# Kernel optimization log

Hardware: AMD Instinct MI355X
Metric: run time of the kernel (lower is better)

The kernel has to match this reference:

```python
import jax, jax.numpy as jnp
import numpy as np

TAU = 0.01          # gumbel_softmax temperature
EPS = 1e-7          # tf.keras.backend.epsilon()
DEPTH = 5
N_NODES = 2 ** DEPTH - 1   # 31 internal nodes
N_LEAVES = 2 ** DEPTH      # 32 leaves


def _build_route():
    # route[l, node + dir*N_NODES] = 1 along the root-to-leaf path of leaf l
    # (same structure old_route_to_new_route produces for a perfect tree)
    route = np.zeros((N_LEAVES, 2 * N_NODES), dtype=np.float32)
    for l in range(N_LEAVES):
        node = 0
        for d in range(DEPTH):
            bit = (l >> (DEPTH - 1 - d)) & 1  # 0 = left, 1 = right
            route[l, node + bit * N_NODES] = 1.0
            node = 2 * node + 1 + bit
    return route


def setup_inputs() -> dict:
    B, F, T = 32768, 128, 100
    key = jax.random.key(0)
    k1, k2, k3, k4 = jax.random.split(key, 4)
    x = jax.random.normal(k1, (B, F), dtype=jnp.float32)
    kernel = jax.random.normal(k2, (T, F, N_NODES), dtype=jnp.float32) * 0.1
    bias = jax.random.normal(k3, (T, N_NODES), dtype=jnp.float32) * 0.1
    leaf = jax.random.normal(k4, (T, N_LEAVES), dtype=jnp.float32)
    route = jnp.asarray(_build_route())  # [L, 2N], shared tree topology
    return {"x": x, "kernel": kernel, "bias": bias, "leaf": leaf, "route": route}


def reference(x, kernel, bias, leaf, route):
    # NodeLayer: matmul(x, concat([K, -K], 1)) + concat([b, -b], 0)
    h = jnp.einsum("bf,tfn->btn", x, kernel) + bias          # [B, T, N]
    h2 = jnp.concatenate([h, -h], axis=-1)                   # [B, T, 2N]
    # activation1: log(clip(sigmoid(clip(h/tau, -32, 32)), eps, 1))
    a1 = jnp.log(jnp.clip(jax.nn.sigmoid(jnp.clip(h2 / TAU, -32.0, 32.0)), EPS, 1.0))
    # route aggregation: sum log-probs along each root->leaf path
    r = jnp.einsum("btm,lm->btl", a1, route)                 # [B, T, L]
    # activation2: exp(clip(., -32, 0)) -> leaf routing probabilities
    probs = jnp.exp(jnp.clip(r, -32.0, 0.0))
    # weight leaf values by route probabilities, sum over leaves and trees
    return jnp.einsum("btl,tl->b", probs, leaf)              # [B] raw GBM output
```

## Files before the change

### kernel.cpp

```cpp
#include <hip/hip_runtime.h>

typedef _Float16 f16x8 __attribute__((ext_vector_type(8)));
typedef float    f32x4 __attribute__((ext_vector_type(4)));
typedef float    f32x2 __attribute__((ext_vector_type(2)));

#define NTREES  100
#define WAVES   8
#define NCH     13
#define BM      32
#define SCALE   144.269504088896f

#define H_OFF   8192
#define LDS_BYTES (H_OFF + WAVES * 4096)

__device__ __forceinline__ float exp2_fast(float v) {
#if __has_builtin(__builtin_amdgcn_exp2f)
  return __builtin_amdgcn_exp2f(v);
#else
  return exp2f(v);
#endif
}

__device__ __forceinline__ void sig2(float z, float& sl, float& sr) {
  z = fmaxf(z, -24.0f);
  float e = exp2_fast(-z);
  sl = __builtin_amdgcn_rcpf(1.0f + e);
  sr = e * sl;
}

__device__ __forceinline__ int node_perm(int sc, float& sg) {
  const int half = sc >> 4, c = sc & 15;
  sg = 1.0f;
  if (c == 0) { if (half) sg = -1.0f; return 0; }
  if (c == 1) return 1 + half;
  if (c < 4)  return 1 + 2 * half + c;
  if (c < 8)  return 3 + 4 * half + c;
  return 7 + 8 * half + c;
}

__global__ void prep_b(const float* __restrict__ kern, const float* __restrict__ bias,
                       unsigned short* __restrict__ bws, float* __restrict__ bias_s) {
  __shared__ float kt[128][33];
  const int t = blockIdx.x, tid = threadIdx.x;
  const float* src = kern + (size_t)t * (128 * 31);
  for (int i = tid; i < 128 * 32; i += 256) {
    const int f = i >> 5, sc = i & 31;
    float sg; const int g = node_perm(sc, sg);
    kt[f][sc] = src[f * 31 + g] * (SCALE * sg);
  }
  if (tid < 32) {
    float sg; const int g = node_perm(tid, sg);
    bias_s[t * 32 + tid] = bias[t * 31 + g] * (SCALE * sg);
  }
  __syncthreads();
  unsigned short* dst = bws + (size_t)t * 4096;
  for (int s = tid; s < 512; s += 256) {
    const int ks = s >> 7, fr = (s >> 6) & 1, lane = s & 63;
    const int n  = (fr << 4) + (lane & 15);
    const int k0 = ks * 32 + ((lane >> 4) << 3);
    f16x8 o;
    #pragma unroll
    for (int j = 0; j < 8; ++j) o[j] = (_Float16)kt[k0 + j][n];
    *(f16x8*)(dst + s * 8) = o;
  }
}

__global__ __launch_bounds__(512, 6) void gbm_main(
    const float* __restrict__ x,
    const unsigned short* __restrict__ bws,
    const float* __restrict__ bias_s,
    const float* __restrict__ leaf,
    float* __restrict__ out)
{
  __shared__ __align__(16) unsigned char lds[LDS_BYTES];
  float* red = (float*)lds;

  const int tid  = threadIdx.x;
  const int lane = tid & 63;
  const int w    = tid >> 6;
  const int rowbase = blockIdx.x * BM;

  {
    const int row = tid >> 4;
    const int k   = (tid & 15) << 3;
    const float* px = x + (size_t)(rowbase + row) * 128 + k;
    float4 v0 = *(const float4*)px;
    float4 v1 = *(const float4*)(px + 4);
    float vals[8] = {v0.x, v0.y, v0.z, v0.w, v1.x, v1.y, v1.z, v1.w};
    f16x8 h8;
    #pragma unroll
    for (int j = 0; j < 8; ++j) h8[j] = (_Float16)vals[j];
    const int frag = ((row >> 4) << 2) + (k >> 5);
    const int lnn  = (row & 15) + (((k >> 3) & 3) << 4);
    *(f16x8*)(lds + (frag * 64 + lnn) * 16) = h8;
  }

  const int abase = lane * 16;
  const int hc = lane & 15, hr = (lane >> 4) << 2;
  int wb[4][2];
  #pragma unroll
  for (int r = 0; r < 4; ++r)
    #pragma unroll
    for (int ct = 0; ct < 2; ++ct)
      wb[r][ct] = H_OFF + (w << 12) + ((hr + r) << 7) +
                  (((ct << 6) + (hc << 2)) ^ (((hr + r) & 7) << 4));
  const int rrow = lane & 31, rhalf = lane >> 5;
  int rb[4];
  #pragma unroll
  for (int g = 0; g < 4; ++g)
    rb[g] = H_OFF + (w << 12) + (rrow << 7) +
            (((rhalf << 6) + (g << 4)) ^ ((rrow & 7) << 4));

  __syncthreads();

  float outAcc = 0.0f;

  for (int c = 0; c < NCH; ++c) {
    const int tree = c * WAVES + w;
    const bool act = tree < NTREES;
    const int tt = act ? tree : (NTREES - 1);

    f16x8 breg[8];
    const unsigned short* bt = bws + (size_t)tt * 4096;
    #pragma unroll
    for (int i = 0; i < 8; ++i)
      breg[i] = *(const f16x8*)(bt + (size_t)i * 512 + lane * 8);

    const float bv0 = bias_s[tt * 32 + hc];
    const float bv1 = bias_s[tt * 32 + 16 + hc];

    if (act) {
      f32x4 acc[2][2] = {};
      __builtin_amdgcn_s_setprio(1);
      #pragma unroll
      for (int ks = 0; ks < 4; ++ks) {
        f16x8 b0 = breg[ks * 2], b1 = breg[ks * 2 + 1];
        #pragma unroll
        for (int rt = 0; rt < 2; ++rt) {
          f16x8 ah = *(const f16x8*)(lds + abase + (rt * 4 + ks) * 1024);
          acc[rt][0] = __builtin_amdgcn_mfma_f32_16x16x32_f16(ah, b0, acc[rt][0], 0, 0, 0);
          acc[rt][1] = __builtin_amdgcn_mfma_f32_16x16x32_f16(ah, b1, acc[rt][1], 0, 0, 0);
        }
      }
      __builtin_amdgcn_s_setprio(0);

      #pragma unroll
      for (int rt = 0; rt < 2; ++rt)
        #pragma unroll
        for (int ct = 0; ct < 2; ++ct)
          #pragma unroll
          for (int r = 0; r < 4; ++r)
            *(float*)(lds + wb[r][ct] + rt * 2048) = acc[rt][ct][r] + (ct ? bv1 : bv0);

      f32x4 h0 = *(const f32x4*)(lds + rb[0]);
      f32x4 h1 = *(const f32x4*)(lds + rb[1]);

      float sl, sr;
      sig2(h0[0], sl, sr);
      const float c0 = sl;
      sig2(h0[1], sl, sr);
      const float a0 = c0 * sl, a1 = c0 * sr;
      sig2(h0[2], sl, sr);
      const float b0_ = a0 * sl, b1_ = a0 * sr;
      sig2(h0[3], sl, sr);
      const float b2_ = a1 * sl, b3_ = a1 * sr;
      float cum[8];
      sig2(h1[0], sl, sr); cum[0] = b0_ * sl; cum[1] = b0_ * sr;
      sig2(h1[1], sl, sr); cum[2] = b1_ * sl; cum[3] = b1_ * sr;
      sig2(h1[2], sl, sr); cum[4] = b2_ * sl; cum[5] = b2_ * sr;
      sig2(h1[3], sl, sr); cum[6] = b3_ * sl; cum[7] = b3_ * sr;

      f32x4 h2 = *(const f32x4*)(lds + rb[2]);
      f32x4 h3 = *(const f32x4*)(lds + rb[3]);
      const f32x2* lp2 = (const f32x2*)(leaf + (size_t)tree * 32 + (rhalf << 4));

      float s = 0.0f;
      #pragma unroll
      for (int i = 0; i < 4; ++i) {
        sig2(h2[i], sl, sr);
        f32x2 lv = lp2[i];
        s = fmaf(cum[i], fmaf(sl, lv[0], sr * lv[1]), s);
      }
      #pragma unroll
      for (int i = 0; i < 4; ++i) {
        sig2(h3[i], sl, sr);
        f32x2 lv = lp2[4 + i];
        s = fmaf(cum[4 + i], fmaf(sl, lv[0], sr * lv[1]), s);
      }
      outAcc += s;
    }
  }

  __syncthreads();
  red[tid] = outAcc;
  __syncthreads();
  if (tid < 32) {
    float s = 0.0f;
    #pragma unroll
    for (int j = 0; j < 16; ++j)
      s += red[j * 32 + tid];
    out[rowbase + tid] = s;
  }
}

extern "C" void kernel_launch(void* const* d_in, const int* in_sizes, int n_in,
                              void* d_out, int out_size, void* d_ws, size_t ws_size,
                              hipStream_t stream) {
  const float* x    = (const float*)d_in[0];
  const float* kern = (const float*)d_in[1];
  const float* bias = (const float*)d_in[2];
  const float* leaf = (const float*)d_in[3];

  unsigned short* bws = (unsigned short*)d_ws;
  float* bias_s = (float*)((unsigned char*)d_ws + 819200);

  prep_b<<<NTREES, 256, 0, stream>>>(kern, bias, bws, bias_s);
  gbm_main<<<32768 / BM, 512, 0, stream>>>(x, bws, bias_s, leaf, (float*)d_out);
}
```

Before: 62.26 us.

## Use 32x32x16 MFMA with bias folded into K and register-resident tree outputs

```diff
diff --git a/kernel.cpp b/kernel.cpp
--- a/kernel.cpp
+++ b/kernel.cpp
@@ -1,17 +1,27 @@
 #include <hip/hip_runtime.h>
 
-typedef _Float16 f16x8 __attribute__((ext_vector_type(8)));
-typedef float    f32x4 __attribute__((ext_vector_type(4)));
-typedef float    f32x2 __attribute__((ext_vector_type(2)));
+typedef _Float16 f16x8  __attribute__((ext_vector_type(8)));
+typedef float    f32x16 __attribute__((ext_vector_type(16)));
+typedef float    f32x4  __attribute__((ext_vector_type(4)));
 
 #define NTREES  100
 #define WAVES   8
 #define NCH     13
 #define BM      32
+#define KS      9
+#define TSTRIDE (KS * 512)
 #define SCALE   144.269504088896f
 
-#define H_OFF   8192
-#define LDS_BYTES (H_OFF + WAVES * 4096)
+__device__ __forceinline__ int node_of_row(int sr, float& sg) {
+  const int h   = (sr >> 2) & 1;
+  const int reg = (sr & 3) + ((sr >> 3) << 2);
+  sg = 1.0f;
+  if (reg == 0) { if (h) sg = -1.0f; return 0; }
+  if (reg == 1) return 1 + h;
+  if (reg < 4)  return 1 + 2 * h + reg;
+  if (reg < 8)  return 3 + 4 * h + reg;
+  return 7 + 8 * h + reg;
+}
 
 __device__ __forceinline__ float exp2_fast(float v) {
 #if __has_builtin(__builtin_amdgcn_exp2f)
@@ -22,57 +32,52 @@
 }
 
 __device__ __forceinline__ void sig2(float z, float& sl, float& sr) {
-  z = fmaxf(z, -24.0f);
   float e = exp2_fast(-z);
   sl = __builtin_amdgcn_rcpf(1.0f + e);
-  sr = e * sl;
-}
-
-__device__ __forceinline__ int node_perm(int sc, float& sg) {
-  const int half = sc >> 4, c = sc & 15;
-  sg = 1.0f;
-  if (c == 0) { if (half) sg = -1.0f; return 0; }
-  if (c == 1) return 1 + half;
-  if (c < 4)  return 1 + 2 * half + c;
-  if (c < 8)  return 3 + 4 * half + c;
-  return 7 + 8 * half + c;
+  sr = 1.0f - sl;
 }
 
 __global__ void prep_b(const float* __restrict__ kern, const float* __restrict__ bias,
-                       unsigned short* __restrict__ bws, float* __restrict__ bias_s) {
-  __shared__ float kt[128][33];
+                       unsigned short* __restrict__ bws) {
+  __shared__ float kt[128][32];
+  __shared__ float bs[32];
   const int t = blockIdx.x, tid = threadIdx.x;
   const float* src = kern + (size_t)t * (128 * 31);
   for (int i = tid; i < 128 * 32; i += 256) {
-    const int f = i >> 5, sc = i & 31;
-    float sg; const int g = node_perm(sc, sg);
-    kt[f][sc] = src[f * 31 + g] * (SCALE * sg);
+    const int f = i >> 5, sr_ = i & 31;
+    float sg; const int g = node_of_row(sr_, sg);
+    kt[f][sr_] = src[f * 31 + g] * (SCALE * sg);
   }
   if (tid < 32) {
-    float sg; const int g = node_perm(tid, sg);
-    bias_s[t * 32 + tid] = bias[t * 31 + g] * (SCALE * sg);
+    float sg; const int g = node_of_row(tid, sg);
+    bs[tid] = bias[t * 31 + g] * (SCALE * sg);
   }
   __syncthreads();
-  unsigned short* dst = bws + (size_t)t * 4096;
-  for (int s = tid; s < 512; s += 256) {
-    const int ks = s >> 7, fr = (s >> 6) & 1, lane = s & 63;
-    const int n  = (fr << 4) + (lane & 15);
-    const int k0 = ks * 32 + ((lane >> 4) << 3);
+  unsigned short* dst = bws + (size_t)t * TSTRIDE;
+  for (int s = tid; s < KS * 64; s += 256) {
+    const int ks = s >> 6, lane = s & 63;
+    const int row = lane & 31;
+    const int k0 = ks * 16 + ((lane >> 5) << 3);
     f16x8 o;
-    #pragma unroll
-    for (int j = 0; j < 8; ++j) o[j] = (_Float16)kt[k0 + j][n];
+    if (ks < 8) {
+      #pragma unroll
+      for (int j = 0; j < 8; ++j) o[j] = (_Float16)kt[k0 + j][row];
+    } else {
+      #pragma unroll
+      for (int j = 0; j < 8; ++j) o[j] = (_Float16)0.0f;
+      if (lane < 32) o[0] = (_Float16)bs[row];
+    }
     *(f16x8*)(dst + s * 8) = o;
   }
 }
 
-__global__ __launch_bounds__(512, 6) void gbm_main(
+__global__ __launch_bounds__(512, 4) void gbm_main(
     const float* __restrict__ x,
     const unsigned short* __restrict__ bws,
-    const float* __restrict__ bias_s,
     const float* __restrict__ leaf,
     float* __restrict__ out)
 {
-  __shared__ __align__(16) unsigned char lds[LDS_BYTES];
+  __shared__ __align__(16) unsigned char lds[KS * 64 * 16];
   float* red = (float*)lds;
 
   const int tid  = threadIdx.x;
@@ -80,113 +85,89 @@
   const int w    = tid >> 6;
   const int rowbase = blockIdx.x * BM;
 
-  {
-    const int row = tid >> 4;
-    const int k   = (tid & 15) << 3;
-    const float* px = x + (size_t)(rowbase + row) * 128 + k;
-    float4 v0 = *(const float4*)px;
-    float4 v1 = *(const float4*)(px + 4);
-    float vals[8] = {v0.x, v0.y, v0.z, v0.w, v1.x, v1.y, v1.z, v1.w};
+  for (int s = tid; s < KS * 64; s += 512) {
+    const int ks = s >> 6, l = s & 63;
     f16x8 h8;
-    #pragma unroll
-    for (int j = 0; j < 8; ++j) h8[j] = (_Float16)vals[j];
-    const int frag = ((row >> 4) << 2) + (k >> 5);
-    const int lnn  = (row & 15) + (((k >> 3) & 3) << 4);
-    *(f16x8*)(lds + (frag * 64 + lnn) * 16) = h8;
+    if (ks < 8) {
+      const int xrow = l & 31;
+      const int k0 = ks * 16 + ((l >> 5) << 3);
+      const float* px = x + (size_t)(rowbase + xrow) * 128 + k0;
+      float4 v0 = *(const float4*)px;
+      float4 v1 = *(const float4*)(px + 4);
+      h8[0] = (_Float16)v0.x; h8[1] = (_Float16)v0.y;
+      h8[2] = (_Float16)v0.z; h8[3] = (_Float16)v0.w;
+      h8[4] = (_Float16)v1.x; h8[5] = (_Float16)v1.y;
+      h8[6] = (_Float16)v1.z; h8[7] = (_Float16)v1.w;
+    } else {
+      #pragma unroll
+      for (int j = 0; j < 8; ++j) h8[j] = (_Float16)0.0f;
+      if (l < 32) h8[0] = (_Float16)1.0f;
+    }
+    *(f16x8*)(lds + s * 16) = h8;
   }
 
-  const int abase = lane * 16;
-  const int hc = lane & 15, hr = (lane >> 4) << 2;
-  int wb[4][2];
-  #pragma unroll
-  for (int r = 0; r < 4; ++r)
+  f16x8 br[KS];
+  {
+    const unsigned short* bt = bws + (size_t)w * TSTRIDE;
     #pragma unroll
-    for (int ct = 0; ct < 2; ++ct)
-      wb[r][ct] = H_OFF + (w << 12) + ((hr + r) << 7) +
-                  (((ct << 6) + (hc << 2)) ^ (((hr + r) & 7) << 4));
-  const int rrow = lane & 31, rhalf = lane >> 5;
-  int rb[4];
-  #pragma unroll
-  for (int g = 0; g < 4; ++g)
-    rb[g] = H_OFF + (w << 12) + (rrow << 7) +
-            (((rhalf << 6) + (g << 4)) ^ ((rrow & 7) << 4));
+    for (int i = 0; i < KS; ++i)
+      br[i] = *(const f16x8*)(bt + (size_t)i * 512 + lane * 8);
+  }
 
   __syncthreads();
 
+  const int h = lane >> 5;
   float outAcc = 0.0f;
 
   for (int c = 0; c < NCH; ++c) {
     const int tree = c * WAVES + w;
     const bool act = tree < NTREES;
-    const int tt = act ? tree : (NTREES - 1);
 
-    f16x8 breg[8];
-    const unsigned short* bt = bws + (size_t)tt * 4096;
-    #pragma unroll
-    for (int i = 0; i < 8; ++i)
-      breg[i] = *(const f16x8*)(bt + (size_t)i * 512 + lane * 8);
+    f32x16 acc = {};
+    if (act) {
+      __builtin_amdgcn_s_setprio(1);
+      #pragma unroll
+      for (int ks = 0; ks < KS; ++ks) {
+        f16x8 bx = *(const f16x8*)(lds + (ks * 64 + lane) * 16);
+        acc = __builtin_amdgcn_mfma_f32_32x32x16_f16(br[ks], bx, acc, 0, 0, 0);
+      }
+      __builtin_amdgcn_s_setprio(0);
+    }
 
-    const float bv0 = bias_s[tt * 32 + hc];
-    const float bv1 = bias_s[tt * 32 + 16 + hc];
+    if ((c + 1) * WAVES + w < NTREES) {
+      const unsigned short* nb = bws + (size_t)((c + 1) * WAVES + w) * TSTRIDE;
+      #pragma unroll
+      for (int i = 0; i < KS; ++i)
+        br[i] = *(const f16x8*)(nb + (size_t)i * 512 + lane * 8);
+    }
 
     if (act) {
-      f32x4 acc[2][2] = {};
-      __builtin_amdgcn_s_setprio(1);
-      #pragma unroll
-      for (int ks = 0; ks < 4; ++ks) {
-        f16x8 b0 = breg[ks * 2], b1 = breg[ks * 2 + 1];
-        #pragma unroll
-        for (int rt = 0; rt < 2; ++rt) {
-          f16x8 ah = *(const f16x8*)(lds + abase + (rt * 4 + ks) * 1024);
-          acc[rt][0] = __builtin_amdgcn_mfma_f32_16x16x32_f16(ah, b0, acc[rt][0], 0, 0, 0);
-          acc[rt][1] = __builtin_amdgcn_mfma_f32_16x16x32_f16(ah, b1, acc[rt][1], 0, 0, 0);
-        }
-      }
-      __builtin_amdgcn_s_setprio(0);
-
-      #pragma unroll
-      for (int rt = 0; rt < 2; ++rt)
-        #pragma unroll
-        for (int ct = 0; ct < 2; ++ct)
-          #pragma unroll
-          for (int r = 0; r < 4; ++r)
-            *(float*)(lds + wb[r][ct] + rt * 2048) = acc[rt][ct][r] + (ct ? bv1 : bv0);
-
-      f32x4 h0 = *(const f32x4*)(lds + rb[0]);
-      f32x4 h1 = *(const f32x4*)(lds + rb[1]);
+      const float* lp = leaf + (size_t)tree * 32 + (h << 4);
+      f32x4 L0 = *(const f32x4*)lp;
+      f32x4 L1 = *(const f32x4*)(lp + 4);
+      f32x4 L2 = *(const f32x4*)(lp + 8);
+      f32x4 L3 = *(const f32x4*)(lp + 12);
 
       float sl, sr;
-      sig2(h0[0], sl, sr);
-      const float c0 = sl;
-      sig2(h0[1], sl, sr);
-      const float a0 = c0 * sl, a1 = c0 * sr;
-      sig2(h0[2], sl, sr);
-      const float b0_ = a0 * sl, b1_ = a0 * sr;
-      sig2(h0[3], sl, sr);
-      const float b2_ = a1 * sl, b3_ = a1 * sr;
+      sig2(acc[0], sl, sr); const float c0 = sl;
+      sig2(acc[1], sl, sr); const float a0 = c0 * sl, a1 = c0 * sr;
+      sig2(acc[2], sl, sr); const float b0 = a0 * sl, b1 = a0 * sr;
+      sig2(acc[3], sl, sr); const float b2 = a1 * sl, b3 = a1 * sr;
       float cum[8];
-      sig2(h1[0], sl, sr); cum[0] = b0_ * sl; cum[1] = b0_ * sr;
-      sig2(h1[1], sl, sr); cum[2] = b1_ * sl; cum[3] = b1_ * sr;
-      sig2(h1[2], sl, sr); cum[4] = b2_ * sl; cum[5] = b2_ * sr;
-      sig2(h1[3], sl, sr); cum[6] = b3_ * sl; cum[7] = b3_ * sr;
-
-      f32x4 h2 = *(const f32x4*)(lds + rb[2]);
-      f32x4 h3 = *(const f32x4*)(lds + rb[3]);
-      const f32x2* lp2 = (const f32x2*)(leaf + (size_t)tree * 32 + (rhalf << 4));
+      sig2(acc[4], sl, sr); cum[0] = b0 * sl; cum[1] = b0 * sr;
+      sig2(acc[5], sl, sr); cum[2] = b1 * sl; cum[3] = b1 * sr;
+      sig2(acc[6], sl, sr); cum[4] = b2 * sl; cum[5] = b2 * sr;
+      sig2(acc[7], sl, sr); cum[6] = b3 * sl; cum[7] = b3 * sr;
 
       float s = 0.0f;
-      #pragma unroll
-      for (int i = 0; i < 4; ++i) {
-        sig2(h2[i], sl, sr);
-        f32x2 lv = lp2[i];
-        s = fmaf(cum[i], fmaf(sl, lv[0], sr * lv[1]), s);
-      }
-      #pragma unroll
-      for (int i = 0; i < 4; ++i) {
-        sig2(h3[i], sl, sr);
-        f32x2 lv = lp2[4 + i];
-        s = fmaf(cum[4 + i], fmaf(sl, lv[0], sr * lv[1]), s);
-      }
+      sig2(acc[8],  sl, sr); s = fmaf(cum[0], fmaf(sl, L0[0], sr * L0[1]), s);
+      sig2(acc[9],  sl, sr); s = fmaf(cum[1], fmaf(sl, L0[2], sr * L0[3]), s);
+      sig2(acc[10], sl, sr); s = fmaf(cum[2], fmaf(sl, L1[0], sr * L1[1]), s);
+      sig2(acc[11], sl, sr); s = fmaf(cum[3], fmaf(sl, L1[2], sr * L1[3]), s);
+      sig2(acc[12], sl, sr); s = fmaf(cum[4], fmaf(sl, L2[0], sr * L2[1]), s);
+      sig2(acc[13], sl, sr); s = fmaf(cum[5], fmaf(sl, L2[2], sr * L2[3]), s);
+      sig2(acc[14], sl, sr); s = fmaf(cum[6], fmaf(sl, L3[0], sr * L3[1]), s);
+      sig2(acc[15], sl, sr); s = fmaf(cum[7], fmaf(sl, L3[2], sr * L3[3]), s);
       outAcc += s;
     }
   }
@@ -212,8 +193,7 @@
   const float* leaf = (const float*)d_in[3];
 
   unsigned short* bws = (unsigned short*)d_ws;
-  float* bias_s = (float*)((unsigned char*)d_ws + 819200);
 
-  prep_b<<<NTREES, 256, 0, stream>>>(kern, bias, bws, bias_s);
-  gbm_main<<<32768 / BM, 512, 0, stream>>>(x, bws, bias_s, leaf, (float*)d_out);
+  prep_b<<<NTREES, 256, 0, stream>>>(kern, bias, bws);
+  gbm_main<<<32768 / BM, 512, 0, stream>>>(x, bws, leaf, (float*)d_out);
 }
```

After: 60.65 us. -2.6%, faster.
